# Optimization experiments

Measured on AMD Instinct MI355X. Metric: run time of the kernel, lower is better.

The kernel has to match this reference:

```python
import jax, jax.numpy as jnp
import numpy as np

EPS = 1e-05


def setup_inputs() -> dict:
    key = jax.random.key(0)
    k1, k2, k3 = jax.random.split(key, 3)
    b, s, n, m = 16, 4096, 1024, 1024
    x = jax.random.normal(k1, (b, s, n), dtype=jnp.float32)
    # torch.rand -> uniform [0,1)
    A = jax.random.uniform(k2, (m, n), dtype=jnp.float32)
    B = jax.random.uniform(k3, (m, n), dtype=jnp.float32)
    return {"x": x, "A": A, "B": B}


def reference(x, A, B):
    # query: project each token with A, then sum over seq -> [b, m]
    query = jnp.einsum('ij,bsj->bi', A, x)  # fused projection + seq-sum
    query = query / (EPS + jnp.linalg.norm(query, axis=1, keepdims=True))
    # keys: [b, s, m], L2-normalized per token
    keys = jnp.einsum('ij,bsj->bsi', B, x)
    keys = keys / (EPS + jnp.linalg.norm(keys, axis=2, keepdims=True))
    # cosine-style similarity (no softmax): [b, s]
    sim = jnp.einsum('bi,bsi->bs', query, keys)
    # weighted sum of raw inputs: [b, n]
    out = jnp.einsum('bs,bsn->bn', sim, x)
    return (out, sim)
```

## Files before the change

### kernel.cpp

```cpp
#include <hip/hip_runtime.h>

#define EPS 1e-5f

typedef __bf16 bf16x8 __attribute__((ext_vector_type(8)));
typedef __bf16 bf16x4 __attribute__((ext_vector_type(4)));
typedef __bf16 bf16x2 __attribute__((ext_vector_type(2)));
typedef float f32x4 __attribute__((ext_vector_type(4)));

static __device__ __forceinline__ unsigned int f2bf(float f) {
    unsigned int u = __builtin_bit_cast(unsigned int, f);
    u = (u + 0x7fffu + ((u >> 16) & 1u)) >> 16;
    return u;
}

static __device__ __forceinline__ void gll16(const void* g, void* l) {
    __builtin_amdgcn_global_load_lds(
        (const __attribute__((address_space(1))) unsigned int*)(unsigned long long)g,
        (__attribute__((address_space(3))) unsigned int*)(unsigned int)(unsigned long long)l,
        16, 0, 0);
}

template <int XBF>
__global__ __launch_bounds__(256) void k_prep(const float* __restrict__ x,
                                              float* __restrict__ xs_part,
                                              unsigned short* __restrict__ xbf) {
    const int b = blockIdx.y, sc = blockIdx.x, tid = threadIdx.x;
    const size_t rowbase = ((size_t)(b * 4096 + sc * 128)) * 1024;
    const float4* src = (const float4*)(x + rowbase) + tid;
    uint2* dst = XBF ? ((uint2*)(xbf + rowbase) + tid) : (uint2*)0;
    float ax = 0.f, ay = 0.f, az = 0.f, aw = 0.f;
    for (int r = 0; r < 128; ++r) {
        float4 v = src[r * 256];
        ax += v.x; ay += v.y; az += v.z; aw += v.w;
        if (XBF) {
            uint2 p;
            p.x = f2bf(v.x) | (f2bf(v.y) << 16);
            p.y = f2bf(v.z) | (f2bf(v.w) << 16);
            dst[r * 256] = p;
        }
    }
    float4 o; o.x = ax; o.y = ay; o.z = az; o.w = aw;
    ((float4*)(xs_part + ((size_t)(b * 32 + sc)) * 1024))[tid] = o;
}

__global__ void k_bconv(const float* __restrict__ B, unsigned short* __restrict__ Bb) {
    const int i = blockIdx.x * 256 + threadIdx.x;
    float4 v = ((const float4*)B)[i];
    uint2 p;
    p.x = f2bf(v.x) | (f2bf(v.y) << 16);
    p.y = f2bf(v.z) | (f2bf(v.w) << 16);
    ((uint2*)Bb)[i] = p;
}

__global__ __launch_bounds__(256) void k_queryf(const float* __restrict__ xs_part,
                                                const float* __restrict__ A,
                                                float* __restrict__ q) {
    __shared__ float xsl[1024];
    const int b = blockIdx.y, g = blockIdx.x, tid = threadIdx.x;
    {
        float4 s4 = {0.f, 0.f, 0.f, 0.f};
        const float4* p = (const float4*)(xs_part + (size_t)b * 32768) + tid;
        for (int sc = 0; sc < 32; ++sc) {
            float4 v = p[sc * 256];
            s4.x += v.x; s4.y += v.y; s4.z += v.z; s4.w += v.w;
        }
        ((float4*)xsl)[tid] = s4;
    }
    __syncthreads();
    const int i = g * 256 + tid;
    const float4* ar = (const float4*)(A + (size_t)i * 1024);
    float acc = 0.f;
    for (int k = 0; k < 256; ++k) {
        float4 a = ar[k], v = ((const float4*)xsl)[k];
        acc += a.x * v.x + a.y * v.y + a.z * v.z + a.w * v.w;
    }
    q[b * 1024 + i] = acc;
}

__global__ __launch_bounds__(256) void k_wf(const float* __restrict__ B,
                                            const float* __restrict__ q,
                                            float* __restrict__ w) {
    __shared__ float ql[1024];
    __shared__ float wsum[4];
    const int b = blockIdx.y, g = blockIdx.x, tid = threadIdx.x;
    float4 v = ((const float4*)(q + (size_t)b * 1024))[tid];
    float ss = v.x * v.x + v.y * v.y + v.z * v.z + v.w * v.w;
    for (int o = 1; o < 64; o <<= 1) ss += __shfl_xor(ss, o);
    if ((tid & 63) == 0) wsum[tid >> 6] = ss;
    __syncthreads();
    const float inv = 1.f / (EPS + sqrtf(wsum[0] + wsum[1] + wsum[2] + wsum[3]));
    float4 n; n.x = v.x * inv; n.y = v.y * inv; n.z = v.z * inv; n.w = v.w * inv;
    ((float4*)ql)[tid] = n;
    __syncthreads();
    const int j = g * 256 + tid;
    float acc = 0.f;
    for (int i = 0; i < 1024; ++i) acc += B[(size_t)i * 1024 + j] * ql[i];
    w[b * 1024 + j] = acc;
}

__global__ __launch_bounds__(512, 2) void k_main2(const unsigned short* __restrict__ xbf,
                                                  const unsigned short* __restrict__ Bb,
                                                  const float* __restrict__ w,
                                                  float* __restrict__ outp,
                                                  float* __restrict__ sim_out) {
    __shared__ __align__(16) union {
        struct { unsigned short Xs[2][256 * 64]; unsigned short Bs[2][256 * 64]; } g;
        unsigned short xt[32 * 1024];
    } S;
    __shared__ float nsq_s[256];
    __shared__ float wlds[1024];
    __shared__ float numer_s[32];
    __shared__ float simv[32];

    const int tid = threadIdx.x;
    const int lane = tid & 63;
    const int l15 = lane & 15, lg = lane >> 4;
    const int w8 = tid >> 6;
    const int wm = w8 >> 2, wn = w8 & 3;
    const int bx = blockIdx.x;
    const size_t tok0 = (size_t)bx * 256;
    const int b = bx >> 4;

    ((float2*)wlds)[tid] = ((const float2*)(w + (size_t)b * 1024))[tid];
    if (tid < 256) nsq_s[tid] = 0.f;

#define STAGE_B(ts_, bf_, it_)                                                            \
    do {                                                                                  \
        const int mt_ = (ts_) >> 4, ks_ = (ts_) & 15;                                     \
        const int g_ = (it_) * 512 + tid;                                                 \
        const int row_ = g_ >> 3, c_ = g_ & 7;                                            \
        gll16(Bb + (size_t)(mt_ * 256 + row_) * 1024 + ks_ * 64 + ((c_ ^ (row_ & 7)) * 8),\
              (char*)S.g.Bs[bf_] + (size_t)((it_) * 512 + (tid & ~63)) * 16);             \
    } while (0)
#define STAGE_X(ts_, bf_, p_)                                                             \
    do {                                                                                  \
        const int ks_ = (ts_) & 15;                                                       \
        const int w_ = tid >> 6;                                                          \
        const int ar0_ = (w_ < 4) ? ((p_) * 32 + w_ * 8) : (128 + (p_) * 32 + (w_ - 4) * 8); \
        const int ar_ = ar0_ + ((tid & 63) >> 3);                                         \
        const int c_ = tid & 7;                                                           \
        gll16(xbf + (tok0 + ar_) * 1024 + ks_ * 64 + ((c_ ^ (ar_ & 7)) * 8),              \
              (char*)S.g.Xs[bf_] + (size_t)ar0_ * 128);                                   \
    } while (0)

    f32x4 acc[8][4];

#pragma unroll
    for (int it = 0; it < 4; ++it) STAGE_B(0, 0, it);
#pragma unroll
    for (int pp = 0; pp < 4; ++pp) STAGE_X(0, 0, pp);
#pragma unroll
    for (int it = 0; it < 4; ++it) STAGE_B(1, 1, it);
#pragma unroll
    for (int pp = 0; pp < 4; ++pp) STAGE_X(1, 1, pp);

    for (int s = 0; s < 64; ++s) {
        const int buf = s & 1;
        if ((s & 15) == 0) {
#pragma unroll
            for (int mi = 0; mi < 8; ++mi)
#pragma unroll
                for (int ni = 0; ni < 4; ++ni) acc[mi][ni] = (f32x4){0.f, 0.f, 0.f, 0.f};
        }
        if (s < 62) asm volatile("s_waitcnt vmcnt(8)" ::: "memory");
        else        asm volatile("s_waitcnt vmcnt(0)" ::: "memory");
        __builtin_amdgcn_s_barrier();

        const char* xb = (const char*)S.g.Xs[buf] + (wm * 128 + l15) * 128;
        const char* bb = (const char*)S.g.Bs[buf] + (wn * 64 + l15) * 128;
        const int sw = (l15 & 7) << 4;
        const bool pre = (s + 2 < 64);

        bf16x8 bq[4][2];
#pragma unroll
        for (int ni = 0; ni < 4; ++ni)
#pragma unroll
            for (int kk = 0; kk < 2; ++kk)
                bq[ni][kk] = *(const bf16x8*)(bb + ni * 16 * 128 + ((kk * 64 + lg * 16) ^ sw));

#pragma unroll
        for (int p = 0; p < 4; ++p) {
            bf16x8 a[2][2];
#pragma unroll
            for (int mi = 0; mi < 2; ++mi)
#pragma unroll
                for (int kk = 0; kk < 2; ++kk)
                    a[mi][kk] = *(const bf16x8*)(xb + (p * 2 + mi) * 16 * 128 +
                                                 ((kk * 64 + lg * 16) ^ sw));
            if (pre) {
                if (p == 1) { STAGE_B(s + 2, buf, 0); STAGE_B(s + 2, buf, 1); STAGE_X(s + 2, buf, 0); }
                if (p == 2) { STAGE_B(s + 2, buf, 2); STAGE_B(s + 2, buf, 3); STAGE_X(s + 2, buf, 1); }
                if (p == 3) { STAGE_X(s + 2, buf, 2); }
            }
            asm volatile("" ::: "memory");
            __builtin_amdgcn_s_barrier();
            __builtin_amdgcn_s_setprio(1);
#pragma unroll
            for (int mi = 0; mi < 2; ++mi)
#pragma unroll
                for (int ni = 0; ni < 4; ++ni)
#pragma unroll
                    for (int kk = 0; kk < 2; ++kk)
                        acc[p * 2 + mi][ni] = __builtin_amdgcn_mfma_f32_16x16x32_bf16(
                            a[mi][kk], bq[ni][kk], acc[p * 2 + mi][ni], 0, 0, 0);
            __builtin_amdgcn_s_setprio(0);
            asm volatile("" ::: "memory");
            __builtin_amdgcn_s_barrier();
        }
        if (pre) STAGE_X(s + 2, buf, 3);

        if ((s & 15) == 15) {
#pragma unroll
            for (int mi = 0; mi < 8; ++mi)
#pragma unroll
                for (int r = 0; r < 4; ++r) {
                    float v = 0.f;
#pragma unroll
                    for (int ni = 0; ni < 4; ++ni) v += acc[mi][ni][r] * acc[mi][ni][r];
                    v += __shfl_xor(v, 1);
                    v += __shfl_xor(v, 2);
                    v += __shfl_xor(v, 4);
                    v += __shfl_xor(v, 8);
                    if (l15 == 0) atomicAdd(&nsq_s[wm * 128 + mi * 16 + lg * 4 + r], v);
                }
        }
    }
#undef STAGE_B
#undef STAGE_X
    __syncthreads();

    float oa0 = 0.f, oa1 = 0.f;
    for (int sub = 0; sub < 8; ++sub) {
#pragma unroll
        for (int it = 0; it < 8; ++it) {
            const int idx = it * 512 + tid;
            const int row = idx >> 7, c = idx & 127;
            gll16(xbf + (tok0 + sub * 32 + row) * 1024 + (c ^ (row & 7)) * 8,
                  (char*)S.xt + (size_t)(it * 512 + (tid & ~63)) * 16);
        }
        asm volatile("s_waitcnt vmcnt(0)" ::: "memory");
        __syncthreads();
        {
            const int t = tid >> 4, kp = tid & 15;
            const char* pt = (const char*)S.xt + t * 2048;
            const int sw2 = (t & 7) << 4;
            float acc2 = 0.f;
#pragma unroll
            for (int j = 0; j < 8; ++j) {
                bf16x8 v = *(const bf16x8*)(pt + ((j * 256 + kp * 16) ^ sw2));
                const float* wp = wlds + j * 128 + kp * 8;
#pragma unroll
                for (int e = 0; e < 8; ++e) acc2 += (float)v[e] * wp[e];
            }
            acc2 += __shfl_xor(acc2, 1);
            acc2 += __shfl_xor(acc2, 2);
            acc2 += __shfl_xor(acc2, 4);
            acc2 += __shfl_xor(acc2, 8);
            if (kp == 0) numer_s[t] = acc2;
        }
        __syncthreads();
        if (tid < 32) {
            float sv = numer_s[tid] / (EPS + sqrtf(nsq_s[sub * 32 + tid]));
            simv[tid] = sv;
            sim_out[tok0 + sub * 32 + tid] = sv;
        }
        __syncthreads();
        {
            const char* lds = (const char*)S.xt;
            const int nb = tid * 4;
#pragma unroll 4
            for (int t = 0; t < 32; ++t) {
                bf16x2 v = *(const bf16x2*)(lds + t * 2048 + (nb ^ ((t & 7) << 4)));
                float sv = simv[t];
                oa0 += sv * (float)v[0];
                oa1 += sv * (float)v[1];
            }
        }
        __syncthreads();
    }
    float2 o; o.x = oa0; o.y = oa1;
    ((float2*)(outp + (size_t)bx * 1024))[tid] = o;
}

__global__ __launch_bounds__(256, 2) void k_nsq_f32(const float* __restrict__ x,
                                                    const unsigned short* __restrict__ Bb,
                                                    float* __restrict__ nsq_g) {
    __shared__ unsigned short Xs[128 * 64];
    __shared__ unsigned short Bs[128 * 64];
    __shared__ float nsq_s[128];

    const int tid = threadIdx.x;
    const int lane = tid & 63;
    const int l15 = lane & 15, lg = lane >> 4;
    const int w = tid >> 6;
    const int wr = w >> 1, wc = w & 1;
    const int st = blockIdx.x * 128;
    const int mh = blockIdx.y;

    float nsq_reg[4][4];
#pragma unroll
    for (int mi = 0; mi < 4; ++mi)
#pragma unroll
        for (int r = 0; r < 4; ++r) nsq_reg[mi][r] = 0.f;

    for (int mti = 0; mti < 4; ++mti) {
        const int mt = mh * 4 + mti;
        f32x4 acc[4][4];
#pragma unroll
        for (int mi = 0; mi < 4; ++mi)
#pragma unroll
            for (int ni = 0; ni < 4; ++ni) acc[mi][ni] = (f32x4){0.f, 0.f, 0.f, 0.f};

        for (int ks = 0; ks < 16; ++ks) {
            __syncthreads();
            {
                const int row = tid >> 1, kh = tid & 1;
                const float* srcx = x + (size_t)(st + row) * 1024 + ks * 64 + kh * 32;
                char* ldsrow = (char*)Xs + row * 128;
                const int sw = (row & 7) << 4;
#pragma unroll
                for (int j = 0; j < 4; ++j) {
                    float4 v0 = ((const float4*)srcx)[j * 2];
                    float4 v1 = ((const float4*)srcx)[j * 2 + 1];
                    uint4 p;
                    p.x = f2bf(v0.x) | (f2bf(v0.y) << 16);
                    p.y = f2bf(v0.z) | (f2bf(v0.w) << 16);
                    p.z = f2bf(v1.x) | (f2bf(v1.y) << 16);
                    p.w = f2bf(v1.z) | (f2bf(v1.w) << 16);
                    *(uint4*)(ldsrow + (((kh * 4 + j) * 16) ^ sw)) = p;
                }
#pragma unroll
                for (int it = 0; it < 4; ++it) {
                    const int idx = it * 256 + tid;
                    const int brow = idx >> 3, c = idx & 7;
                    char* baseB = (char*)Bs + (size_t)(it * 256 + (tid & ~63)) * 16;
                    gll16(Bb + (size_t)(mt * 128 + brow) * 1024 + ks * 64 + (c ^ (brow & 7)) * 8,
                          baseB);
                }
            }
            __syncthreads();

            const char* xb = (const char*)Xs + (wr * 64 + l15) * 128;
            const char* bb = (const char*)Bs + (wc * 64 + l15) * 128;
            const int sw = (l15 & 7) << 4;
#pragma unroll
            for (int kk = 0; kk < 2; ++kk) {
                const int ob = (kk * 64 + lg * 16) ^ sw;
                bf16x8 a[4], bq[4];
#pragma unroll
                for (int mi = 0; mi < 4; ++mi) a[mi] = *(const bf16x8*)(xb + mi * 2048 + ob);
#pragma unroll
                for (int ni = 0; ni < 4; ++ni) bq[ni] = *(const bf16x8*)(bb + ni * 2048 + ob);
#pragma unroll
                for (int mi = 0; mi < 4; ++mi)
#pragma unroll
                    for (int ni = 0; ni < 4; ++ni)
                        acc[mi][ni] = __builtin_amdgcn_mfma_f32_16x16x32_bf16(
                            a[mi], bq[ni], acc[mi][ni], 0, 0, 0);
            }
        }
#pragma unroll
        for (int mi = 0; mi < 4; ++mi)
#pragma unroll
            for (int ni = 0; ni < 4; ++ni)
#pragma unroll
                for (int r = 0; r < 4; ++r)
                    nsq_reg[mi][r] += acc[mi][ni][r] * acc[mi][ni][r];
    }

    if (tid < 128) nsq_s[tid] = 0.f;
    __syncthreads();
#pragma unroll
    for (int mi = 0; mi < 4; ++mi)
#pragma unroll
        for (int r = 0; r < 4; ++r) {
            float v = nsq_reg[mi][r];
            v += __shfl_xor(v, 1);
            v += __shfl_xor(v, 2);
            v += __shfl_xor(v, 4);
            v += __shfl_xor(v, 8);
            if (l15 == 0) atomicAdd(&nsq_s[wr * 64 + mi * 16 + lg * 4 + r], v);
        }
    __syncthreads();
    if (tid < 128) nsq_g[(size_t)mh * 65536 + st + tid] = nsq_s[tid];
}

__global__ __launch_bounds__(256, 2) void k_finish0(
    const float* __restrict__ x, const float* __restrict__ w,
    const float* __restrict__ nsq_g, float* __restrict__ outp,
    float* __restrict__ sim_out) {
    __shared__ __align__(16) unsigned short xt[32 * 1024];
    __shared__ float numer[32];
    __shared__ float simv[32];

    const int tid = threadIdx.x;
    const int bs = blockIdx.x;
    const int b = bs >> 7, s0 = (bs & 127) * 32;
    const size_t tok0 = (size_t)b * 4096 + s0;

    const float4* src = (const float4*)(x + tok0 * 1024) + tid;
    char* lds = (char*)xt;
    for (int r = 0; r < 32; ++r) {
        float4 v = src[r * 256];
        uint2 p;
        p.x = f2bf(v.x) | (f2bf(v.y) << 16);
        p.y = f2bf(v.z) | (f2bf(v.w) << 16);
        *(uint2*)(lds + r * 2048 + ((tid * 8) ^ ((r & 7) << 4))) = p;
    }
    __syncthreads();

    {
        const int t = tid >> 3, kp = tid & 7;
        const float* wb = w + (size_t)b * 1024 + kp * 128;
        const char* pt = (const char*)xt + t * 2048;
        const int sw2 = (t & 7) << 4;
        float acc = 0.f;
#pragma unroll
        for (int j = 0; j < 16; ++j) {
            const int kb = (kp * 128 + j * 8) * 2;
            bf16x8 v = *(const bf16x8*)(pt + (kb ^ sw2));
#pragma unroll
            for (int e = 0; e < 8; ++e) acc += (float)v[e] * wb[j * 8 + e];
        }
        acc += __shfl_xor(acc, 1);
        acc += __shfl_xor(acc, 2);
        acc += __shfl_xor(acc, 4);
        if (kp == 0) numer[t] = acc;
    }
    __syncthreads();

    if (tid < 32) {
        float nt = nsq_g[tok0 + tid] + nsq_g[65536 + tok0 + tid];
        float s = numer[tid] / (EPS + sqrtf(nt));
        simv[tid] = s;
        sim_out[tok0 + tid] = s;
    }
    __syncthreads();

    {
        const int n0 = tid * 4;
        float a0 = 0.f, a1 = 0.f, a2 = 0.f, a3 = 0.f;
        const char* p = (const char*)xt;
#pragma unroll 4
        for (int t = 0; t < 32; ++t) {
            int byte = t * 2048 + ((n0 * 2) ^ ((t & 7) << 4));
            bf16x4 v = *(const bf16x4*)(p + byte);
            float s = simv[t];
            a0 += s * (float)v[0];
            a1 += s * (float)v[1];
            a2 += s * (float)v[2];
            a3 += s * (float)v[3];
        }
        float4 o; o.x = a0; o.y = a1; o.z = a2; o.w = a3;
        ((float4*)(outp + (size_t)bs * 1024))[tid] = o;
    }
}

template <int NT>
__global__ void k_outred(const float* __restrict__ outp, float* __restrict__ out) {
    const int b = blockIdx.y, j = blockIdx.x * 256 + threadIdx.x;
    const float* p = outp + (size_t)b * NT * 1024 + j;
    float s = 0.f;
    for (int t = 0; t < NT; ++t) s += p[t * 1024];
    out[b * 1024 + j] = s;
}

extern "C" void kernel_launch(void* const* d_in, const int* in_sizes, int n_in,
                              void* d_out, int out_size, void* d_ws, size_t ws_size,
                              hipStream_t stream) {
    const float* x = (const float*)d_in[0];
    const float* A = (const float*)d_in[1];
    const float* B = (const float*)d_in[2];
    float* out = (float*)d_out;
    float* sim = out + 16 * 1024;
    float* ws = (float*)d_ws;
    float* xs_part = ws;
    float* q = ws + 540672;
    float* wv = ws + 557056;
    float* nsq = ws + 573440;
    float* outp = ws + 704512;
    unsigned short* Bb = (unsigned short*)(ws + 2801664);
    unsigned short* xbf = (unsigned short*)(ws + 3325952);
    const bool xb = ws_size >= (size_t)(3325952 + 33554432) * 4;

    if (xb) k_prep<1><<<dim3(32, 16), 256, 0, stream>>>(x, xs_part, xbf);
    else    k_prep<0><<<dim3(32, 16), 256, 0, stream>>>(x, xs_part, (unsigned short*)0);
    k_bconv<<<1024, 256, 0, stream>>>(B, Bb);
    k_queryf<<<dim3(4, 16), 256, 0, stream>>>(xs_part, A, q);
    k_wf<<<dim3(4, 16), 256, 0, stream>>>(B, q, wv);
    if (xb) {
        k_main2<<<256, 512, 0, stream>>>(xbf, Bb, wv, outp, sim);
        k_outred<16><<<dim3(4, 16), 256, 0, stream>>>(outp, out);
    } else {
        k_nsq_f32<<<dim3(512, 2), 256, 0, stream>>>(x, Bb, nsq);
        k_finish0<<<2048, 256, 0, stream>>>(x, wv, nsq, outp, sim);
        k_outred<128><<<dim3(4, 16), 256, 0, stream>>>(outp, out);
    }
}
```

Before: 300.7 us.

## Restructure main GEMM staging and double-buffer the epilogue x tiles

The main loop drops the per-subphase interleaved prefetch and the barrier around every MFMA group. It now runs all MFMAs under one priority raise, then issues a single combined X+B stage for step s+2 after one barrier. The epilogue that rereads x tiles for the weighted sum now uses two LDS buffers, so the next 32-token tile loads while the current one is consumed, and the __syncthreads calls become raw barriers with lgkmcnt waits. This aims to cut barrier count and hide epilogue load latency. The union doubles to 128KB, about the same size as the GEMM buffers, and the coarser prefetch placement may overlap less well with compute.

```diff
diff --git a/kernel.cpp b/kernel.cpp
--- a/kernel.cpp
+++ b/kernel.cpp
@@ -105,7 +105,7 @@
                                                   float* __restrict__ sim_out) {
     __shared__ __align__(16) union {
         struct { unsigned short Xs[2][256 * 64]; unsigned short Bs[2][256 * 64]; } g;
-        unsigned short xt[32 * 1024];
+        unsigned short xt2[2][32 * 1024];
     } S;
     __shared__ float nsq_s[256];
     __shared__ float wlds[1024];
@@ -123,36 +123,26 @@
 
     ((float2*)wlds)[tid] = ((const float2*)(w + (size_t)b * 1024))[tid];
     if (tid < 256) nsq_s[tid] = 0.f;
-
-#define STAGE_B(ts_, bf_, it_)                                                            \
-    do {                                                                                  \
-        const int mt_ = (ts_) >> 4, ks_ = (ts_) & 15;                                     \
-        const int g_ = (it_) * 512 + tid;                                                 \
-        const int row_ = g_ >> 3, c_ = g_ & 7;                                            \
-        gll16(Bb + (size_t)(mt_ * 256 + row_) * 1024 + ks_ * 64 + ((c_ ^ (row_ & 7)) * 8),\
-              (char*)S.g.Bs[bf_] + (size_t)((it_) * 512 + (tid & ~63)) * 16);             \
+    __syncthreads();
+
+#define STAGE(s_, buf_)                                                                  \
+    do {                                                                                 \
+        const int mt_ = (s_) >> 4, ks_ = (s_) & 15;                                      \
+        _Pragma("unroll") for (int it = 0; it < 4; ++it) {                               \
+            const int g_ = it * 512 + tid;                                               \
+            const int row_ = g_ >> 3, c_ = g_ & 7;                                       \
+            const int csw_ = (c_ ^ (row_ & 7)) * 8;                                      \
+            gll16(xbf + (tok0 + row_) * 1024 + ks_ * 64 + csw_,                          \
+                  (char*)S.g.Xs[buf_] + (size_t)(it * 512 + (tid & ~63)) * 16);          \
+            gll16(Bb + (size_t)(mt_ * 256 + row_) * 1024 + ks_ * 64 + csw_,              \
+                  (char*)S.g.Bs[buf_] + (size_t)(it * 512 + (tid & ~63)) * 16);          \
+        }                                                                                \
     } while (0)
-#define STAGE_X(ts_, bf_, p_)                                                             \
-    do {                                                                                  \
-        const int ks_ = (ts_) & 15;                                                       \
-        const int w_ = tid >> 6;                                                          \
-        const int ar0_ = (w_ < 4) ? ((p_) * 32 + w_ * 8) : (128 + (p_) * 32 + (w_ - 4) * 8); \
-        const int ar_ = ar0_ + ((tid & 63) >> 3);                                         \
-        const int c_ = tid & 7;                                                           \
-        gll16(xbf + (tok0 + ar_) * 1024 + ks_ * 64 + ((c_ ^ (ar_ & 7)) * 8),              \
-              (char*)S.g.Xs[bf_] + (size_t)ar0_ * 128);                                   \
-    } while (0)
 
     f32x4 acc[8][4];
 
-#pragma unroll
-    for (int it = 0; it < 4; ++it) STAGE_B(0, 0, it);
-#pragma unroll
-    for (int pp = 0; pp < 4; ++pp) STAGE_X(0, 0, pp);
-#pragma unroll
-    for (int it = 0; it < 4; ++it) STAGE_B(1, 1, it);
-#pragma unroll
-    for (int pp = 0; pp < 4; ++pp) STAGE_X(1, 1, pp);
+    STAGE(0, 0);
+    STAGE(1, 1);
 
     for (int s = 0; s < 64; ++s) {
         const int buf = s & 1;
@@ -169,7 +159,6 @@
         const char* xb = (const char*)S.g.Xs[buf] + (wm * 128 + l15) * 128;
         const char* bb = (const char*)S.g.Bs[buf] + (wn * 64 + l15) * 128;
         const int sw = (l15 & 7) << 4;
-        const bool pre = (s + 2 < 64);
 
         bf16x8 bq[4][2];
 #pragma unroll
@@ -178,6 +167,7 @@
             for (int kk = 0; kk < 2; ++kk)
                 bq[ni][kk] = *(const bf16x8*)(bb + ni * 16 * 128 + ((kk * 64 + lg * 16) ^ sw));
 
+        __builtin_amdgcn_s_setprio(1);
 #pragma unroll
         for (int p = 0; p < 4; ++p) {
             bf16x8 a[2][2];
@@ -187,14 +177,6 @@
                 for (int kk = 0; kk < 2; ++kk)
                     a[mi][kk] = *(const bf16x8*)(xb + (p * 2 + mi) * 16 * 128 +
                                                  ((kk * 64 + lg * 16) ^ sw));
-            if (pre) {
-                if (p == 1) { STAGE_B(s + 2, buf, 0); STAGE_B(s + 2, buf, 1); STAGE_X(s + 2, buf, 0); }
-                if (p == 2) { STAGE_B(s + 2, buf, 2); STAGE_B(s + 2, buf, 3); STAGE_X(s + 2, buf, 1); }
-                if (p == 3) { STAGE_X(s + 2, buf, 2); }
-            }
-            asm volatile("" ::: "memory");
-            __builtin_amdgcn_s_barrier();
-            __builtin_amdgcn_s_setprio(1);
 #pragma unroll
             for (int mi = 0; mi < 2; ++mi)
 #pragma unroll
@@ -203,11 +185,13 @@
                     for (int kk = 0; kk < 2; ++kk)
                         acc[p * 2 + mi][ni] = __builtin_amdgcn_mfma_f32_16x16x32_bf16(
                             a[mi][kk], bq[ni][kk], acc[p * 2 + mi][ni], 0, 0, 0);
-            __builtin_amdgcn_s_setprio(0);
-            asm volatile("" ::: "memory");
-            __builtin_amdgcn_s_barrier();
-        }
-        if (pre) STAGE_X(s + 2, buf, 3);
+        }
+        __builtin_amdgcn_s_setprio(0);
+
+        asm volatile("" ::: "memory");
+        __builtin_amdgcn_s_barrier();
+        asm volatile("" ::: "memory");
+        if (s + 2 < 64) STAGE(s + 2, buf);
 
         if ((s & 15) == 15) {
 #pragma unroll
@@ -225,24 +209,34 @@
                 }
         }
     }
-#undef STAGE_B
-#undef STAGE_X
-    __syncthreads();
+#undef STAGE
+
+#define STAGE_SUB(sub_, bf_)                                                             \
+    do {                                                                                 \
+        _Pragma("unroll") for (int it = 0; it < 8; ++it) {                               \
+            const int idx_ = it * 512 + tid;                                             \
+            const int row_ = idx_ >> 7, c_ = idx_ & 127;                                 \
+            gll16(xbf + (tok0 + (sub_) * 32 + row_) * 1024 + ((c_ ^ (row_ & 7)) * 8),    \
+                  (char*)S.xt2[bf_] + (size_t)(it * 512 + (tid & ~63)) * 16);            \
+        }                                                                                \
+    } while (0)
+
+    STAGE_SUB(0, 0);
+    asm volatile("s_waitcnt lgkmcnt(0)" ::: "memory");
+    __builtin_amdgcn_s_barrier();
 
     float oa0 = 0.f, oa1 = 0.f;
     for (int sub = 0; sub < 8; ++sub) {
-#pragma unroll
-        for (int it = 0; it < 8; ++it) {
-            const int idx = it * 512 + tid;
-            const int row = idx >> 7, c = idx & 127;
-            gll16(xbf + (tok0 + sub * 32 + row) * 1024 + (c ^ (row & 7)) * 8,
-                  (char*)S.xt + (size_t)(it * 512 + (tid & ~63)) * 16);
-        }
-        asm volatile("s_waitcnt vmcnt(0)" ::: "memory");
-        __syncthreads();
+        const int cur = sub & 1;
+        if (sub < 7) STAGE_SUB(sub + 1, cur ^ 1);
+        if (sub < 7) asm volatile("s_waitcnt vmcnt(8)" ::: "memory");
+        else         asm volatile("s_waitcnt vmcnt(0)" ::: "memory");
+        __builtin_amdgcn_s_barrier();
+
+        const char* xt = (const char*)S.xt2[cur];
         {
             const int t = tid >> 4, kp = tid & 15;
-            const char* pt = (const char*)S.xt + t * 2048;
+            const char* pt = xt + t * 2048;
             const int sw2 = (t & 7) << 4;
             float acc2 = 0.f;
 #pragma unroll
@@ -258,26 +252,31 @@
             acc2 += __shfl_xor(acc2, 8);
             if (kp == 0) numer_s[t] = acc2;
         }
-        __syncthreads();
+        asm volatile("s_waitcnt lgkmcnt(0)" ::: "memory");
+        __builtin_amdgcn_s_barrier();
+
         if (tid < 32) {
             float sv = numer_s[tid] / (EPS + sqrtf(nsq_s[sub * 32 + tid]));
             simv[tid] = sv;
             sim_out[tok0 + sub * 32 + tid] = sv;
         }
-        __syncthreads();
+        asm volatile("s_waitcnt lgkmcnt(0)" ::: "memory");
+        __builtin_amdgcn_s_barrier();
+
         {
-            const char* lds = (const char*)S.xt;
             const int nb = tid * 4;
 #pragma unroll 4
             for (int t = 0; t < 32; ++t) {
-                bf16x2 v = *(const bf16x2*)(lds + t * 2048 + (nb ^ ((t & 7) << 4)));
+                bf16x2 v = *(const bf16x2*)(xt + t * 2048 + (nb ^ ((t & 7) << 4)));
                 float sv = simv[t];
                 oa0 += sv * (float)v[0];
                 oa1 += sv * (float)v[1];
             }
         }
-        __syncthreads();
-    }
+        asm volatile("s_waitcnt lgkmcnt(0)" ::: "memory");
+        __builtin_amdgcn_s_barrier();
+    }
+#undef STAGE_SUB
     float2 o; o.x = oa0; o.y = oa1;
     ((float2*)(outp + (size_t)bx * 1024))[tid] = o;
 }
```

New measurement: 303.8 us. Within noise of the previous version (+1.1%).
